# Performance work log

Hardware: AMD Instinct MI355X
Metric: run time of the kernel (lower is better)

Reference implementation:

```python
import jax, jax.numpy as jnp
import numpy as np
from jax import lax

# ---- model dims ----
NTOKEN = 60697
D_MODEL = 512
NLAYERS = 4
D_STATE = 16
D_CONV = 4
EXPAND = 2
D_INNER = EXPAND * D_MODEL      # 1024
DT_RANK = (D_MODEL + 15) // 16  # 32 (ceil(d_model/16), mamba default)
B_SZ = 4
SEQ = 2048
EPS = 1e-5


def setup_inputs() -> dict:
    key = jax.random.key(0)
    ks = jax.random.split(key, 16)
    s = 0.02
    src = jax.random.randint(ks[0], (B_SZ, SEQ), 0, NTOKEN)
    src_key_padding_mask = jnp.ones((B_SZ, SEQ), dtype=bool)
    emb_w = jax.random.normal(ks[1], (NTOKEN, D_MODEL), jnp.float32) * s
    enc_ln_w = jnp.ones((D_MODEL,), jnp.float32)
    enc_ln_b = jnp.zeros((D_MODEL,), jnp.float32)
    ln_w = jnp.ones((NLAYERS, D_MODEL), jnp.float32)
    ln_b = jnp.zeros((NLAYERS, D_MODEL), jnp.float32)
    in_proj_w = jax.random.normal(ks[2], (NLAYERS, 2 * D_INNER, D_MODEL), jnp.float32) * s
    conv_w = jax.random.normal(ks[3], (NLAYERS, D_INNER, D_CONV), jnp.float32) * 0.1
    conv_b = jnp.zeros((NLAYERS, D_INNER), jnp.float32)
    x_proj_w = jax.random.normal(ks[4], (NLAYERS, DT_RANK + 2 * D_STATE, D_INNER), jnp.float32) * s
    dt_proj_w = jax.random.normal(ks[5], (NLAYERS, D_INNER, DT_RANK), jnp.float32) * (DT_RANK ** -0.5)
    dt_proj_b = jax.random.uniform(ks[6], (NLAYERS, D_INNER), jnp.float32, -4.0, -2.0)
    # S4D real init: A = -[1..d_state], stored as log
    A_log = jnp.log(jnp.broadcast_to(jnp.arange(1, D_STATE + 1, dtype=jnp.float32),
                                     (NLAYERS, D_INNER, D_STATE)))
    D_skip = jnp.ones((NLAYERS, D_INNER), jnp.float32)
    out_proj_w = jax.random.normal(ks[7], (NLAYERS, D_MODEL, D_INNER), jnp.float32) * s / np.sqrt(NLAYERS)
    normf_w = jnp.ones((D_MODEL,), jnp.float32)
    normf_b = jnp.zeros((D_MODEL,), jnp.float32)
    return {
        'src': src, 'src_key_padding_mask': src_key_padding_mask,
        'emb_w': emb_w, 'enc_ln_w': enc_ln_w, 'enc_ln_b': enc_ln_b,
        'ln_w': ln_w, 'ln_b': ln_b, 'in_proj_w': in_proj_w,
        'conv_w': conv_w, 'conv_b': conv_b, 'x_proj_w': x_proj_w,
        'dt_proj_w': dt_proj_w, 'dt_proj_b': dt_proj_b,
        'A_log': A_log, 'D_skip': D_skip, 'out_proj_w': out_proj_w,
        'normf_w': normf_w, 'normf_b': normf_b,
    }


def _layer_norm(x, w, b, eps=EPS):
    mu = jnp.mean(x, axis=-1, keepdims=True)
    var = jnp.mean(jnp.square(x - mu), axis=-1, keepdims=True)
    return (x - mu) * lax.rsqrt(var + eps) * w + b


def _mamba_mixer(h, in_w, cw, cb, xw, dtw, dtb, A_log, D_skip, ow):
    B, L, _ = h.shape
    xz = h @ in_w.T                                   # [B,L,2*d_inner]
    x, z = jnp.split(xz, 2, axis=-1)
    # causal depthwise conv1d, kernel D_CONV
    xt = x.swapaxes(1, 2)                             # [B,d_inner,L]
    xp = jnp.pad(xt, ((0, 0), (0, 0), (D_CONV - 1, 0)))
    conv = cb[None, :, None]
    for k in range(D_CONV):
        conv = conv + cw[:, k][None, :, None] * xp[:, :, k:k + L]
    x = jax.nn.silu(conv).swapaxes(1, 2)              # [B,L,d_inner]
    xdbl = x @ xw.T                                   # [B,L,dt_rank+2*d_state]
    dt = jax.nn.softplus(xdbl[..., :DT_RANK] @ dtw.T + dtb)      # [B,L,d_inner]
    Bm = xdbl[..., DT_RANK:DT_RANK + D_STATE]                    # [B,L,d_state]
    Cm = xdbl[..., DT_RANK + D_STATE:]                           # [B,L,d_state]
    A = -jnp.exp(A_log)                               # [d_inner,d_state]

    def step(hst, inp):
        dt_t, b_t, c_t, x_t = inp                     # [B,d_inner],[B,d_state],[B,d_state],[B,d_inner]
        dA = jnp.exp(dt_t[..., None] * A)             # [B,d_inner,d_state]
        hst = dA * hst + (dt_t * x_t)[..., None] * b_t[:, None, :]
        y_t = jnp.einsum('bds,bs->bd', hst, c_t)
        return hst, y_t

    xs = (dt.swapaxes(0, 1), Bm.swapaxes(0, 1), Cm.swapaxes(0, 1), x.swapaxes(0, 1))
    h0 = jnp.zeros((B, D_INNER, D_STATE), dtype=h.dtype)
    _, ys = lax.scan(step, h0, xs)                    # ys: [L,B,d_inner]
    y = ys.swapaxes(0, 1) + x * D_skip
    y = y * jax.nn.silu(z)
    return y @ ow.T


def reference(src, src_key_padding_mask, emb_w, enc_ln_w, enc_ln_b, ln_w, ln_b,
              in_proj_w, conv_w, conv_b, x_proj_w, dt_proj_w, dt_proj_b,
              A_log, D_skip, out_proj_w, normf_w, normf_b):
    # GeneEncoder: embedding -> LayerNorm (dropout = identity in eval)
    hidden = _layer_norm(emb_w[src], enc_ln_w, enc_ln_b)
    residual = None
    for i in range(NLAYERS):  # prenorm Mamba Blocks
        residual = hidden if residual is None else hidden + residual
        hidden = _mamba_mixer(_layer_norm(residual, ln_w[i], ln_b[i]),
                              in_proj_w[i], conv_w[i], conv_b[i], x_proj_w[i],
                              dt_proj_w[i], dt_proj_b[i], A_log[i], D_skip[i],
                              out_proj_w[i])
    residual = hidden + residual
    return _layer_norm(residual, normf_w, normf_b)
```

## Files before the change

kernel.cpp:

```cpp
#include <hip/hip_runtime.h>
#include <hip/hip_bf16.h>
#include <math.h>

#define NTOKEN 60697
#define D_MODEL 512
#define NLAYERS 4
#define D_STATE 16
#define D_CONV 4
#define D_INNER 1024
#define DT_RANK 32
#define B_SZ 4
#define SEQ 2048
#define EPS 1e-5f
#define NROWS (B_SZ * SEQ)
#define CHUNK 128
#define NCHUNK (SEQ / CHUNK)

typedef __bf16 bf16_t;
typedef __attribute__((ext_vector_type(8))) __bf16 bfx8;
typedef __attribute__((ext_vector_type(4))) __bf16 bfx4;
typedef __attribute__((ext_vector_type(4))) float f32x4;


__device__ __forceinline__ float fast_sigmoid(float x) {
    return 1.0f / (1.0f + __expf(-x));
}
__device__ __forceinline__ float silu(float x) {
    return x * fast_sigmoid(x);
}
__device__ __forceinline__ float softplus_f(float x) {
    return (x > 20.0f) ? x : log1pf(__expf(x));
}

__device__ __forceinline__ void gload_lds16(const void* g, void* l) {
    __builtin_amdgcn_global_load_lds(
        (const __attribute__((address_space(1))) unsigned int*)g,
        (__attribute__((address_space(3))) unsigned int*)l, 16, 0, 0);
}

template <int CTRL>
__device__ __forceinline__ float dpp_fetch(float x) {
    int xi = __builtin_bit_cast(int, x);
    int yi = __builtin_amdgcn_update_dpp(0, xi, CTRL, 0xF, 0xF, true);
    return __builtin_bit_cast(float, yi);
}
__device__ __forceinline__ float dpp_sum16(float p) {
    p += dpp_fetch<0xB1>(p);
    p += dpp_fetch<0x4E>(p);
    p += dpp_fetch<0x141>(p);
    p += dpp_fetch<0x140>(p);
    return p;
}

__device__ __forceinline__ float blk_reduce_sum(float x, float* sbuf) {
#pragma unroll
    for (int m = 32; m >= 1; m >>= 1) x += __shfl_xor(x, m);
    int wid = threadIdx.x >> 6;
    if ((threadIdx.x & 63) == 0) sbuf[wid] = x;
    __syncthreads();
    float t = sbuf[0] + sbuf[1] + sbuf[2] + sbuf[3];
    __syncthreads();
    return t;
}

__global__ __launch_bounds__(256) void cast_bf16_kernel(
    const float* __restrict__ in, bf16_t* __restrict__ out, size_t n)
{
    size_t stride = (size_t)gridDim.x * 256 * 4;
    for (size_t i = ((size_t)blockIdx.x * 256 + threadIdx.x) * 4; i < n; i += stride) {
        float4 v = *reinterpret_cast<const float4*>(in + i);
        bfx4 o;
        o[0] = (bf16_t)v.x; o[1] = (bf16_t)v.y;
        o[2] = (bf16_t)v.z; o[3] = (bf16_t)v.w;
        *reinterpret_cast<bfx4*>(out + i) = o;
    }
}


__global__ __launch_bounds__(256) void embed_ln_kernel(
    const int* __restrict__ src, const float* __restrict__ emb,
    const float* __restrict__ w, const float* __restrict__ b,
    float* __restrict__ R)
{
    __shared__ float sbuf[4];
    int row = blockIdx.x;
    int tok = src[row];
    const float* e = emb + (size_t)tok * D_MODEL;
    int c0 = threadIdx.x, c1 = threadIdx.x + 256;
    float v0 = e[c0], v1 = e[c1];
    float mu = blk_reduce_sum(v0 + v1, sbuf) * (1.0f / D_MODEL);
    float d0 = v0 - mu, d1 = v1 - mu;
    float var = blk_reduce_sum(d0 * d0 + d1 * d1, sbuf) * (1.0f / D_MODEL);
    float rs = rsqrtf(var + EPS);
    size_t base = (size_t)row * D_MODEL;
    R[base + c0] = d0 * rs * w[c0] + b[c0];
    R[base + c1] = d1 * rs * w[c1] + b[c1];
}

__global__ __launch_bounds__(256) void add_ln_kernel(
    float* __restrict__ R, const float* __restrict__ Hadd,
    const float* __restrict__ w, const float* __restrict__ b,
    float* __restrict__ out, bf16_t* __restrict__ outb)
{
    __shared__ float sbuf[4];
    size_t base = (size_t)blockIdx.x * D_MODEL;
    int c0 = threadIdx.x, c1 = c0 + 256;
    float v0 = R[base + c0], v1 = R[base + c1];
    if (Hadd) {
        v0 += Hadd[base + c0];
        v1 += Hadd[base + c1];
        R[base + c0] = v0;
        R[base + c1] = v1;
    }
    float mu = blk_reduce_sum(v0 + v1, sbuf) * (1.0f / D_MODEL);
    float d0 = v0 - mu, d1 = v1 - mu;
    float var = blk_reduce_sum(d0 * d0 + d1 * d1, sbuf) * (1.0f / D_MODEL);
    float rs = rsqrtf(var + EPS);
    float o0 = d0 * rs * w[c0] + b[c0];
    float o1 = d1 * rs * w[c1] + b[c1];
    if (out) {
        out[base + c0] = o0;
        out[base + c1] = o1;
    }
    if (outb) {
        outb[base + c0] = (bf16_t)o0;
        outb[base + c1] = (bf16_t)o1;
    }
}

template <int EPI>
__global__ __launch_bounds__(256) void gemm_bf16_nt(
    const bf16_t* __restrict__ A, const bf16_t* __restrict__ B,
    float* __restrict__ C, int ldc, int K, const float* __restrict__ bias,
    const unsigned short* __restrict__ xcb_u16,
    unsigned short* __restrict__ dtx_u16,
    bf16_t* __restrict__ Cxb, bf16_t* __restrict__ Czb)
{
    __shared__ bf16_t As[128 * 32];
    __shared__ bf16_t Bs[128 * 32];
    int tid = threadIdx.x;
    int lane = tid & 63, wid = tid >> 6;
    int m0 = blockIdx.y * 128, n0 = blockIdx.x * 128;
    int wm = (wid >> 1) * 64, wn = (wid & 1) * 64;
    int c_lo = lane & 15;
    int khalf = lane >> 4;

    f32x4 acc[4][4];
#pragma unroll
    for (int i = 0; i < 4; i++)
#pragma unroll
        for (int j = 0; j < 4; j++)
            acc[i][j] = (f32x4){0.f, 0.f, 0.f, 0.f};

    for (int k0 = 0; k0 < K; k0 += 32) {
#pragma unroll
        for (int i = 0; i < 2; i++) {
            int c = i * 256 + tid;
            int row = c >> 2;
            int cb = (c & 3) * 16;
            int ldsoff = (i * 256 + wid * 64) * 16;
            gload_lds16((const char*)A + ((size_t)(m0 + row) * K + k0) * 2 + cb,
                        (char*)As + ldsoff);
            gload_lds16((const char*)B + ((size_t)(n0 + row) * K + k0) * 2 + cb,
                        (char*)Bs + ldsoff);
        }
        __syncthreads();

        bfx8 af[4], bfr[4];
#pragma unroll
        for (int i = 0; i < 4; i++) {
            af[i]  = *reinterpret_cast<const bfx8*>(As + (wm + i * 16 + c_lo) * 32 + khalf * 8);
            bfr[i] = *reinterpret_cast<const bfx8*>(Bs + (wn + i * 16 + c_lo) * 32 + khalf * 8);
        }
#pragma unroll
        for (int i = 0; i < 4; i++)
#pragma unroll
            for (int j = 0; j < 4; j++)
                acc[i][j] = __builtin_amdgcn_mfma_f32_16x16x32_bf16(af[i], bfr[j], acc[i][j], 0, 0, 0);
        __syncthreads();
    }

#pragma unroll
    for (int i = 0; i < 4; i++) {
#pragma unroll
        for (int j = 0; j < 4; j++) {
            int row0 = m0 + wm + i * 16 + khalf * 4;
            int col = n0 + wn + j * 16 + c_lo;
#pragma unroll
            for (int r = 0; r < 4; r++) {
                int row = row0 + r;
                float v = acc[i][j][r];
                if (EPI == 0) {
                    C[(size_t)row * ldc + col] = v;
                } else if (EPI == 2) {
                    v = softplus_f(v + bias[col]);
                    unsigned int db = (unsigned int)__builtin_bit_cast(unsigned short, (bf16_t)v);
                    unsigned int xb = (unsigned int)xcb_u16[(size_t)row * D_INNER + col];
                    *(unsigned int*)(dtx_u16 + (size_t)row * 2048 + 2 * col) = db | (xb << 16);
                } else if (EPI == 3) {
                    if (col < D_INNER) Cxb[(size_t)row * D_INNER + col] = (bf16_t)v;
                    else               Czb[(size_t)row * D_INNER + col - D_INNER] = (bf16_t)v;
                }
            }
        }
    }
}

__global__ __launch_bounds__(128) void gemm_xp_bf16(
    const bf16_t* __restrict__ A, const bf16_t* __restrict__ Bmat,
    bf16_t* __restrict__ XDlow, float* __restrict__ BCX, int K)
{
    __shared__ bf16_t As[64 * 32];
    __shared__ bf16_t Bs[64 * 32];
    int tid = threadIdx.x;
    int lane = tid & 63, w = tid >> 6;
    int m0 = blockIdx.x * 64;
    int wr0 = w * 32;
    int c_lo = lane & 15;
    int khalf = lane >> 4;

    f32x4 acc[2][4];
#pragma unroll
    for (int i = 0; i < 2; i++)
#pragma unroll
        for (int j = 0; j < 4; j++)
            acc[i][j] = (f32x4){0.f, 0.f, 0.f, 0.f};

    for (int k0 = 0; k0 < K; k0 += 32) {
#pragma unroll
        for (int call = 0; call < 2; call++) {
            int c = call * 128 + tid;
            int base = (call * 128 + w * 64) * 16;
            gload_lds16((const char*)A + ((size_t)(m0 + (c >> 2)) * K + k0) * 2 + (c & 3) * 16,
                        (char*)As + base);
            gload_lds16((const char*)Bmat + ((size_t)(c >> 2) * K + k0) * 2 + (c & 3) * 16,
                        (char*)Bs + base);
        }
        __syncthreads();

        bfx8 af[2], bfr[4];
#pragma unroll
        for (int i = 0; i < 2; i++)
            af[i] = *reinterpret_cast<const bfx8*>(As + (wr0 + i * 16 + c_lo) * 32 + khalf * 8);
#pragma unroll
        for (int j = 0; j < 4; j++)
            bfr[j] = *reinterpret_cast<const bfx8*>(Bs + (j * 16 + c_lo) * 32 + khalf * 8);
#pragma unroll
        for (int i = 0; i < 2; i++)
#pragma unroll
            for (int j = 0; j < 4; j++)
                acc[i][j] = __builtin_amdgcn_mfma_f32_16x16x32_bf16(af[i], bfr[j], acc[i][j], 0, 0, 0);
        __syncthreads();
    }

#pragma unroll
    for (int i = 0; i < 2; i++)
#pragma unroll
        for (int j = 0; j < 4; j++) {
            int row0 = m0 + wr0 + i * 16 + khalf * 4;
            int col = j * 16 + c_lo;
#pragma unroll
            for (int r = 0; r < 4; r++) {
                int row = row0 + r;
                float v = acc[i][j][r];
                if (col < DT_RANK) {
                    XDlow[(size_t)row * DT_RANK + col] = (bf16_t)v;
                } else {
                    int c2 = col - DT_RANK;
                    BCX[(size_t)row * 32 + 2 * (c2 & 15) + (c2 >> 4)] = v;
                }
            }
        }
}

__global__ __launch_bounds__(256) void conv_silu_kernel(
    const bf16_t* __restrict__ Xrawb, const float* __restrict__ cw,
    const float* __restrict__ cb, bf16_t* __restrict__ XCb)
{
    size_t gid = (size_t)blockIdx.x * 256 + threadIdx.x;
    int d = (int)(gid & (D_INNER - 1));
    size_t bt = gid >> 10;
    int t = (int)(bt & (SEQ - 1));
    float acc = cb[d];
#pragma unroll
    for (int k = 0; k < D_CONV; k++) {
        int tt = t + k - (D_CONV - 1);
        if (tt >= 0)
            acc += cw[d * D_CONV + k] * (float)Xrawb[(bt + (size_t)(k - (D_CONV - 1))) * D_INNER + d];
    }
    XCb[gid] = (bf16_t)silu(acc);
}

__device__ __forceinline__ void scan_stage(
    char* base, const unsigned int* __restrict__ DTXb,
    const float* __restrict__ BCX, size_t r0, int d0, int w, int lane)
{
    if (w < 2) {
        int cdt = w * 64 + lane;
        gload_lds16((const char*)DTXb + ((r0 + (cdt >> 2)) * 1024 + d0) * 4 + (cdt & 3) * 16,
                    base + w * 1024);
        int cbc = 128 + w * 64;
        gload_lds16((const char*)BCX + (r0 + ((cbc + lane) >> 3)) * 128 + ((cbc + lane) & 7) * 16,
                    base + 2048 + cbc * 16);
    } else {
        int cbc = (w - 2) * 64;
        gload_lds16((const char*)BCX + (r0 + ((cbc + lane) >> 3)) * 128 + ((cbc + lane) & 7) * 16,
                    base + 2048 + cbc * 16);
    }
}

__global__ __launch_bounds__(256) void scan_pA_kernel(
    const unsigned int* __restrict__ DTXb, const float* __restrict__ BCX,
    const float* __restrict__ A_log,
    float* __restrict__ DcB, float* __restrict__ UcB)
{
    __shared__ __align__(16) char lds[2][6144];
    const int tid = threadIdx.x;
    const int w = tid >> 6, lane = tid & 63;
    const int s = tid & 15, dl = tid >> 4;
    const int b = blockIdx.x >> 6;
    const int d0 = (blockIdx.x & 63) * 16;
    const int c = blockIdx.y;
    const int d = d0 + dl;
    const float Av = -__expf(A_log[d * D_STATE + s]);
    const size_t bbase = (size_t)b * SEQ;
    const int tstart = c * CHUNK;

    float h = 0.f, cum = 0.f;
    scan_stage(lds[0], DTXb, BCX, bbase + tstart, d0, w, lane);
    __syncthreads();
    int cur = 0;
    for (int t0 = 0; t0 < CHUNK; t0 += 32) {
        if (t0 + 32 < CHUNK)
            scan_stage(lds[cur ^ 1], DTXb, BCX, bbase + tstart + t0 + 32, d0, w, lane);
        const char* L = lds[cur];
#pragma unroll
        for (int kk = 0; kk < 32; kk++) {
            unsigned int pk = *(const unsigned int*)(L + kk * 64 + dl * 4);
            float dtv = __builtin_bit_cast(float, pk << 16);
            float xv  = __builtin_bit_cast(float, pk & 0xFFFF0000u);
            float bv  = *(const float*)(L + 2048 + kk * 128 + s * 8);
            float e = __expf(dtv * Av);
            h = fmaf(e, h, dtv * xv * bv);
            cum += dtv;
        }
        __syncthreads();
        cur ^= 1;
    }
    size_t cb64 = ((size_t)c * B_SZ + b) * D_INNER + d;
    UcB[cb64 * 16 + s] = h;
    if (s == 0) DcB[cb64] = cum;
}

__global__ __launch_bounds__(256) void scan_p2_kernel(
    const float* __restrict__ A_log, const float* __restrict__ DcB,
    const float* __restrict__ UcB, float* __restrict__ HcB)
{
    int tid = threadIdx.x;
    int s = tid & 15, dl = tid >> 4;
    int chain = blockIdx.x * 16 + dl;
    int b = chain >> 10, d = chain & 1023;
    float Av = -__expf(A_log[d * D_STATE + s]);
    float Hv = 0.f;
    for (int c = 0; c < NCHUNK; c++) {
        size_t base = ((size_t)c * B_SZ + b) * D_INNER + d;
        HcB[base * 16 + s] = Hv;
        Hv = __expf(Av * DcB[base]) * Hv + UcB[base * 16 + s];
    }
}

__global__ __launch_bounds__(256) void scan_pB_kernel(
    const unsigned int* __restrict__ DTXb, const float* __restrict__ BCX,
    const float* __restrict__ HcB, const float* __restrict__ A_log,
    const bf16_t* __restrict__ Zbufb, const float* __restrict__ Dskip,
    bf16_t* __restrict__ XCb)
{
    __shared__ __align__(16) char lds[2][6144];
    __shared__ float ytile[32][17];
    const int tid = threadIdx.x;
    const int w = tid >> 6, lane = tid & 63;
    const int s = tid & 15, dl = tid >> 4;
    const int b = blockIdx.x >> 6;
    const int d0 = (blockIdx.x & 63) * 16;
    const int c = blockIdx.y;
    const int d = d0 + dl;
    const float Av = -__expf(A_log[d * D_STATE + s]);
    const size_t bbase = (size_t)b * SEQ;
    const int tstart = c * CHUNK;

    float h = HcB[(((size_t)c * B_SZ + b) * D_INNER + d) * 16 + s];

    const int tl  = tid >> 3;
    const int dlo = (tid * 2) & 15;
    const float dsk0 = Dskip[d0 + dlo];
    const float dsk1 = Dskip[d0 + dlo + 1];

    scan_stage(lds[0], DTXb, BCX, bbase + tstart, d0, w, lane);
    __syncthreads();
    int cur = 0;
    for (int t0 = 0; t0 < CHUNK; t0 += 32) {
        if (t0 + 32 < CHUNK)
            scan_stage(lds[cur ^ 1], DTXb, BCX, bbase + tstart + t0 + 32, d0, w, lane);
        const char* L = lds[cur];
#pragma unroll
        for (int half = 0; half < 2; half++) {
            float yhold = 0.f;
#pragma unroll
            for (int k = 0; k < 16; k++) {
                int kk = half * 16 + k;
                unsigned int pk = *(const unsigned int*)(L + kk * 64 + dl * 4);
                float dtv = __builtin_bit_cast(float, pk << 16);
                float xv  = __builtin_bit_cast(float, pk & 0xFFFF0000u);
                float2 bc = *(const float2*)(L + 2048 + kk * 128 + s * 8);
                float e = __expf(dtv * Av);
                h = fmaf(e, h, dtv * xv * bc.x);
                float p = dpp_sum16(h * bc.y);
                if (s == k) yhold = p;
            }
            ytile[half * 16 + s][dl] = yhold;
        }
        __syncthreads();

        {
            int t = tstart + t0 + tl;
            size_t row = (bbase + t) * (size_t)D_INNER + d0 + dlo;
            float y0 = ytile[tl][dlo];
            float y1 = ytile[tl][dlo + 1];
            unsigned int xw = *(const unsigned int*)(XCb + row);
            float x0 = __builtin_bit_cast(float, xw << 16);
            float x1 = __builtin_bit_cast(float, xw & 0xFFFF0000u);
            unsigned int zw = *(const unsigned int*)(Zbufb + row);
            float z0 = __builtin_bit_cast(float, zw << 16);
            float z1 = __builtin_bit_cast(float, zw & 0xFFFF0000u);
            float g0 = (y0 + x0 * dsk0) * silu(z0);
            float g1 = (y1 + x1 * dsk1) * silu(z1);
            unsigned int o = (unsigned int)__builtin_bit_cast(unsigned short, (bf16_t)g0)
                           | ((unsigned int)__builtin_bit_cast(unsigned short, (bf16_t)g1) << 16);
            *(unsigned int*)(XCb + row) = o;
        }
        __syncthreads();
        cur ^= 1;
    }
}


extern "C" void kernel_launch(void* const* d_in, const int* in_sizes, int n_in,
                              void* d_out, int out_size, void* d_ws, size_t ws_size,
                              hipStream_t stream) {
    const int*   src       = (const int*)d_in[0];
    const float* emb_w     = (const float*)d_in[2];
    const float* enc_ln_w  = (const float*)d_in[3];
    const float* enc_ln_b  = (const float*)d_in[4];
    const float* ln_w      = (const float*)d_in[5];
    const float* ln_b      = (const float*)d_in[6];
    const float* in_proj_w = (const float*)d_in[7];
    const float* conv_w    = (const float*)d_in[8];
    const float* conv_b    = (const float*)d_in[9];
    const float* x_proj_w  = (const float*)d_in[10];
    const float* dt_proj_w = (const float*)d_in[11];
    const float* dt_proj_b = (const float*)d_in[12];
    const float* A_log     = (const float*)d_in[13];
    const float* D_skip    = (const float*)d_in[14];
    const float* out_proj_w= (const float*)d_in[15];
    const float* normf_w   = (const float*)d_in[16];
    const float* normf_b   = (const float*)d_in[17];
    float* out = (float*)d_out;

    float* R    = (float*)d_ws;
    float* H    = R    + (size_t)NROWS * D_MODEL;
    float* BCX  = H    + (size_t)NROWS * D_MODEL;
    float* DcB  = BCX  + (size_t)NROWS * 32;
    float* UcB  = DcB  + (size_t)NCHUNK * B_SZ * D_INNER;
    float* HcB  = UcB  + (size_t)NCHUNK * B_SZ * D_INNER * D_STATE;
    bf16_t* Hb    = (bf16_t*)(HcB + (size_t)NCHUNK * B_SZ * D_INNER * D_STATE);
    bf16_t* Xrawb = Hb    + (size_t)NROWS * D_MODEL;
    bf16_t* Zbufb = Xrawb + (size_t)NROWS * D_INNER;
    bf16_t* XCb   = Zbufb + (size_t)NROWS * D_INNER;
    bf16_t* XDlow = XCb   + (size_t)NROWS * D_INNER;
    unsigned short* DTXb = (unsigned short*)(XDlow + (size_t)NROWS * DT_RANK);
    bf16_t* Wib   = (bf16_t*)(DTXb + (size_t)NROWS * 2048);
    bf16_t* Wob   = Wib   + (size_t)NLAYERS * 2 * D_INNER * D_MODEL;
    bf16_t* xpb   = Wob   + (size_t)NLAYERS * D_MODEL * D_INNER;
    bf16_t* dtwb  = xpb   + (size_t)NLAYERS * 64 * D_INNER;

    cast_bf16_kernel<<<2048, 256, 0, stream>>>(in_proj_w, Wib, (size_t)NLAYERS * 2 * D_INNER * D_MODEL);
    cast_bf16_kernel<<<2048, 256, 0, stream>>>(out_proj_w, Wob, (size_t)NLAYERS * D_MODEL * D_INNER);
    cast_bf16_kernel<<<256, 256, 0, stream>>>(x_proj_w, xpb, (size_t)NLAYERS * 64 * D_INNER);
    cast_bf16_kernel<<<128, 256, 0, stream>>>(dt_proj_w, dtwb, (size_t)NLAYERS * D_INNER * DT_RANK);

    embed_ln_kernel<<<NROWS, 256, 0, stream>>>(src, emb_w, enc_ln_w, enc_ln_b, R);

    for (int L = 0; L < NLAYERS; L++) {
        const float* AlogL = A_log + (size_t)L * D_INNER * D_STATE;

        add_ln_kernel<<<NROWS, 256, 0, stream>>>(
            R, (L == 0) ? nullptr : H, ln_w + L * D_MODEL, ln_b + L * D_MODEL,
            nullptr, Hb);

        gemm_bf16_nt<3><<<dim3(16, 64), 256, 0, stream>>>(
            Hb, Wib + (size_t)L * 2 * D_INNER * D_MODEL, nullptr, 0, D_MODEL,
            nullptr, nullptr, nullptr, Xrawb, Zbufb);

        conv_silu_kernel<<<(NROWS * D_INNER) / 256, 256, 0, stream>>>(
            Xrawb, conv_w + (size_t)L * D_INNER * D_CONV, conv_b + (size_t)L * D_INNER, XCb);

        gemm_xp_bf16<<<NROWS / 64, 128, 0, stream>>>(
            XCb, xpb + (size_t)L * 64 * D_INNER, XDlow, BCX, D_INNER);

        gemm_bf16_nt<2><<<dim3(8, 64), 256, 0, stream>>>(
            XDlow, dtwb + (size_t)L * D_INNER * DT_RANK, nullptr, 0, DT_RANK,
            dt_proj_b + (size_t)L * D_INNER, (const unsigned short*)XCb, DTXb,
            nullptr, nullptr);

        scan_pA_kernel<<<dim3(B_SZ * 64, NCHUNK), 256, 0, stream>>>(
            (const unsigned int*)DTXb, BCX, AlogL, DcB, UcB);
        scan_p2_kernel<<<256, 256, 0, stream>>>(AlogL, DcB, UcB, HcB);
        scan_pB_kernel<<<dim3(B_SZ * 64, NCHUNK), 256, 0, stream>>>(
            (const unsigned int*)DTXb, BCX, HcB, AlogL, Zbufb,
            D_skip + (size_t)L * D_INNER, XCb);

        gemm_bf16_nt<0><<<dim3(4, 64), 256, 0, stream>>>(
            XCb, Wob + (size_t)L * D_MODEL * D_INNER, H, D_MODEL, D_INNER,
            nullptr, nullptr, nullptr, nullptr, nullptr);
    }

    add_ln_kernel<<<NROWS, 256, 0, stream>>>(R, H, normf_w, normf_b, out, nullptr);
}
```

Measured before the change: 1.091 ms.

## Pack scan inputs as bf16 row-pairs, precompute dt*x, use exp2

The dt epilogue now stores dt and dt*x as bf16 pairs, interleaved by row pairs. The x_proj epilogue stores B and C as bf16 pairs in the same row-pair layout instead of fp32. The scan kernels stage 64 timesteps per LDS buffer with one 16-byte load per thread, read two timesteps per uint2, and use raw v_exp_f32 with A pre-scaled by log2e. This is meant to halve B/C traffic, cut per-step multiplies and exp cost, and make staging simpler. In exchange B, C and dt*x lose precision by being rounded to bf16 before the recurrence.

```diff
diff --git a/kernel.cpp b/kernel.cpp
--- a/kernel.cpp
+++ b/kernel.cpp
@@ -15,6 +15,7 @@
 #define NROWS (B_SZ * SEQ)
 #define CHUNK 128
 #define NCHUNK (SEQ / CHUNK)
+#define LOG2E 1.44269504f
 
 typedef __bf16 bf16_t;
 typedef __attribute__((ext_vector_type(8))) __bf16 bfx8;
@@ -30,6 +31,20 @@
 }
 __device__ __forceinline__ float softplus_f(float x) {
     return (x > 20.0f) ? x : log1pf(__expf(x));
+}
+__device__ __forceinline__ float exp2_fast(float x) {
+    float r;
+    asm("v_exp_f32 %0, %1" : "=v"(r) : "v"(x));
+    return r;
+}
+__device__ __forceinline__ unsigned int bf16bits(float v) {
+    return (unsigned int)__builtin_bit_cast(unsigned short, (bf16_t)v);
+}
+__device__ __forceinline__ float lo16f(unsigned int u) {
+    return __builtin_bit_cast(float, u << 16);
+}
+__device__ __forceinline__ float hi16f(unsigned int u) {
+    return __builtin_bit_cast(float, u & 0xFFFF0000u);
 }
 
 __device__ __forceinline__ void gload_lds16(const void* g, void* l) {
@@ -133,7 +148,7 @@
     const bf16_t* __restrict__ A, const bf16_t* __restrict__ B,
     float* __restrict__ C, int ldc, int K, const float* __restrict__ bias,
     const unsigned short* __restrict__ xcb_u16,
-    unsigned short* __restrict__ dtx_u16,
+    unsigned int* __restrict__ dtx_u32,
     bf16_t* __restrict__ Cxb, bf16_t* __restrict__ Czb)
 {
     __shared__ bf16_t As[128 * 32];
@@ -194,9 +209,9 @@
                     C[(size_t)row * ldc + col] = v;
                 } else if (EPI == 2) {
                     v = softplus_f(v + bias[col]);
-                    unsigned int db = (unsigned int)__builtin_bit_cast(unsigned short, (bf16_t)v);
-                    unsigned int xb = (unsigned int)xcb_u16[(size_t)row * D_INNER + col];
-                    *(unsigned int*)(dtx_u16 + (size_t)row * 2048 + 2 * col) = db | (xb << 16);
+                    float xf = lo16f((unsigned int)xcb_u16[(size_t)row * D_INNER + col]);
+                    unsigned int u = bf16bits(v) | (bf16bits(v * xf) << 16);
+                    dtx_u32[(size_t)(row >> 1) * 2048 + col * 2 + (row & 1)] = u;
                 } else if (EPI == 3) {
                     if (col < D_INNER) Cxb[(size_t)row * D_INNER + col] = (bf16_t)v;
                     else               Czb[(size_t)row * D_INNER + col - D_INNER] = (bf16_t)v;
@@ -208,7 +223,7 @@
 
 __global__ __launch_bounds__(128) void gemm_xp_bf16(
     const bf16_t* __restrict__ A, const bf16_t* __restrict__ Bmat,
-    bf16_t* __restrict__ XDlow, float* __restrict__ BCX, int K)
+    bf16_t* __restrict__ XDlow, unsigned int* __restrict__ BCb, int K)
 {
     __shared__ bf16_t As[64 * 32];
     __shared__ bf16_t Bs[64 * 32];
@@ -254,23 +269,17 @@
     }
 
 #pragma unroll
-    for (int i = 0; i < 2; i++)
-#pragma unroll
-        for (int j = 0; j < 4; j++) {
-            int row0 = m0 + wr0 + i * 16 + khalf * 4;
-            int col = j * 16 + c_lo;
-#pragma unroll
-            for (int r = 0; r < 4; r++) {
-                int row = row0 + r;
-                float v = acc[i][j][r];
-                if (col < DT_RANK) {
-                    XDlow[(size_t)row * DT_RANK + col] = (bf16_t)v;
-                } else {
-                    int c2 = col - DT_RANK;
-                    BCX[(size_t)row * 32 + 2 * (c2 & 15) + (c2 >> 4)] = v;
-                }
-            }
-        }
+    for (int i = 0; i < 2; i++) {
+        int row0 = m0 + wr0 + i * 16 + khalf * 4;
+#pragma unroll
+        for (int r = 0; r < 4; r++) {
+            int row = row0 + r;
+            XDlow[(size_t)row * DT_RANK + c_lo]      = (bf16_t)acc[i][0][r];
+            XDlow[(size_t)row * DT_RANK + 16 + c_lo] = (bf16_t)acc[i][1][r];
+            unsigned int u = bf16bits(acc[i][2][r]) | (bf16bits(acc[i][3][r]) << 16);
+            BCb[(size_t)(row >> 1) * 32 + c_lo * 2 + (row & 1)] = u;
+        }
+    }
 }
 
 __global__ __launch_bounds__(256) void conv_silu_kernel(
@@ -291,58 +300,54 @@
     XCb[gid] = (bf16_t)silu(acc);
 }
 
-__device__ __forceinline__ void scan_stage(
-    char* base, const unsigned int* __restrict__ DTXb,
-    const float* __restrict__ BCX, size_t r0, int d0, int w, int lane)
-{
-    if (w < 2) {
-        int cdt = w * 64 + lane;
-        gload_lds16((const char*)DTXb + ((r0 + (cdt >> 2)) * 1024 + d0) * 4 + (cdt & 3) * 16,
-                    base + w * 1024);
-        int cbc = 128 + w * 64;
-        gload_lds16((const char*)BCX + (r0 + ((cbc + lane) >> 3)) * 128 + ((cbc + lane) & 7) * 16,
-                    base + 2048 + cbc * 16);
-    } else {
-        int cbc = (w - 2) * 64;
-        gload_lds16((const char*)BCX + (r0 + ((cbc + lane) >> 3)) * 128 + ((cbc + lane) & 7) * 16,
-                    base + 2048 + cbc * 16);
-    }
+__device__ __forceinline__ void scan_stage64(
+    char* base, const unsigned int* __restrict__ DTXp,
+    const unsigned int* __restrict__ BCp, size_t rowpair0, int d0, int tid)
+{
+    gload_lds16(DTXp + (rowpair0 + (size_t)(tid >> 3)) * 2048 + d0 * 2 + (tid & 7) * 4,
+                base + tid * 16);
+    gload_lds16(BCp + rowpair0 * 32 + tid * 4, base + 4096 + tid * 16);
 }
 
 __global__ __launch_bounds__(256) void scan_pA_kernel(
-    const unsigned int* __restrict__ DTXb, const float* __restrict__ BCX,
+    const unsigned int* __restrict__ DTXb, const unsigned int* __restrict__ BCb,
     const float* __restrict__ A_log,
     float* __restrict__ DcB, float* __restrict__ UcB)
 {
-    __shared__ __align__(16) char lds[2][6144];
+    __shared__ __align__(16) char lds[2][8192];
     const int tid = threadIdx.x;
-    const int w = tid >> 6, lane = tid & 63;
     const int s = tid & 15, dl = tid >> 4;
     const int b = blockIdx.x >> 6;
     const int d0 = (blockIdx.x & 63) * 16;
     const int c = blockIdx.y;
     const int d = d0 + dl;
-    const float Av = -__expf(A_log[d * D_STATE + s]);
+    const float Av2 = -__expf(A_log[d * D_STATE + s]) * LOG2E;
     const size_t bbase = (size_t)b * SEQ;
     const int tstart = c * CHUNK;
 
     float h = 0.f, cum = 0.f;
-    scan_stage(lds[0], DTXb, BCX, bbase + tstart, d0, w, lane);
+    scan_stage64(lds[0], DTXb, BCb, (bbase + tstart) >> 1, d0, tid);
     __syncthreads();
     int cur = 0;
-    for (int t0 = 0; t0 < CHUNK; t0 += 32) {
-        if (t0 + 32 < CHUNK)
-            scan_stage(lds[cur ^ 1], DTXb, BCX, bbase + tstart + t0 + 32, d0, w, lane);
+    for (int t0 = 0; t0 < CHUNK; t0 += 64) {
+        if (t0 + 64 < CHUNK)
+            scan_stage64(lds[cur ^ 1], DTXb, BCb, (bbase + tstart + t0 + 64) >> 1, d0, tid);
         const char* L = lds[cur];
 #pragma unroll
-        for (int kk = 0; kk < 32; kk++) {
-            unsigned int pk = *(const unsigned int*)(L + kk * 64 + dl * 4);
-            float dtv = __builtin_bit_cast(float, pk << 16);
-            float xv  = __builtin_bit_cast(float, pk & 0xFFFF0000u);
-            float bv  = *(const float*)(L + 2048 + kk * 128 + s * 8);
-            float e = __expf(dtv * Av);
-            h = fmaf(e, h, dtv * xv * bv);
-            cum += dtv;
+        for (int kk2 = 0; kk2 < 32; kk2++) {
+            uint2 dp = *(const uint2*)(L + kk2 * 128 + dl * 8);
+            uint2 bp = *(const uint2*)(L + 4096 + kk2 * 128 + s * 8);
+#pragma unroll
+            for (int j = 0; j < 2; j++) {
+                unsigned int pk = j ? dp.y : dp.x;
+                unsigned int bk = j ? bp.y : bp.x;
+                float dtv = lo16f(pk);
+                float ux  = hi16f(pk);
+                float bv  = lo16f(bk);
+                float e = exp2_fast(dtv * Av2);
+                h = fmaf(e, h, ux * bv);
+                cum += dtv;
+            }
         }
         __syncthreads();
         cur ^= 1;
@@ -370,21 +375,20 @@
 }
 
 __global__ __launch_bounds__(256) void scan_pB_kernel(
-    const unsigned int* __restrict__ DTXb, const float* __restrict__ BCX,
+    const unsigned int* __restrict__ DTXb, const unsigned int* __restrict__ BCb,
     const float* __restrict__ HcB, const float* __restrict__ A_log,
     const bf16_t* __restrict__ Zbufb, const float* __restrict__ Dskip,
     bf16_t* __restrict__ XCb)
 {
-    __shared__ __align__(16) char lds[2][6144];
+    __shared__ __align__(16) char lds[2][8192];
     __shared__ float ytile[32][17];
     const int tid = threadIdx.x;
-    const int w = tid >> 6, lane = tid & 63;
     const int s = tid & 15, dl = tid >> 4;
     const int b = blockIdx.x >> 6;
     const int d0 = (blockIdx.x & 63) * 16;
     const int c = blockIdx.y;
     const int d = d0 + dl;
-    const float Av = -__expf(A_log[d * D_STATE + s]);
+    const float Av2 = -__expf(A_log[d * D_STATE + s]) * LOG2E;
     const size_t bbase = (size_t)b * SEQ;
     const int tstart = c * CHUNK;
 
@@ -395,50 +399,56 @@
     const float dsk0 = Dskip[d0 + dlo];
     const float dsk1 = Dskip[d0 + dlo + 1];
 
-    scan_stage(lds[0], DTXb, BCX, bbase + tstart, d0, w, lane);
+    scan_stage64(lds[0], DTXb, BCb, (bbase + tstart) >> 1, d0, tid);
     __syncthreads();
     int cur = 0;
-    for (int t0 = 0; t0 < CHUNK; t0 += 32) {
-        if (t0 + 32 < CHUNK)
-            scan_stage(lds[cur ^ 1], DTXb, BCX, bbase + tstart + t0 + 32, d0, w, lane);
+    for (int t0 = 0; t0 < CHUNK; t0 += 64) {
+        if (t0 + 64 < CHUNK)
+            scan_stage64(lds[cur ^ 1], DTXb, BCb, (bbase + tstart + t0 + 64) >> 1, d0, tid);
         const char* L = lds[cur];
 #pragma unroll
-        for (int half = 0; half < 2; half++) {
-            float yhold = 0.f;
-#pragma unroll
-            for (int k = 0; k < 16; k++) {
-                int kk = half * 16 + k;
-                unsigned int pk = *(const unsigned int*)(L + kk * 64 + dl * 4);
-                float dtv = __builtin_bit_cast(float, pk << 16);
-                float xv  = __builtin_bit_cast(float, pk & 0xFFFF0000u);
-                float2 bc = *(const float2*)(L + 2048 + kk * 128 + s * 8);
-                float e = __expf(dtv * Av);
-                h = fmaf(e, h, dtv * xv * bc.x);
-                float p = dpp_sum16(h * bc.y);
-                if (s == k) yhold = p;
+        for (int g = 0; g < 2; g++) {
+#pragma unroll
+            for (int half = 0; half < 2; half++) {
+                float yhold = 0.f;
+#pragma unroll
+                for (int k8 = 0; k8 < 8; k8++) {
+                    int kk2 = g * 16 + half * 8 + k8;
+                    uint2 dp = *(const uint2*)(L + kk2 * 128 + dl * 8);
+                    uint2 bp = *(const uint2*)(L + 4096 + kk2 * 128 + s * 8);
+#pragma unroll
+                    for (int j = 0; j < 2; j++) {
+                        unsigned int pk = j ? dp.y : dp.x;
+                        unsigned int bk = j ? bp.y : bp.x;
+                        float dtv = lo16f(pk);
+                        float ux  = hi16f(pk);
+                        float bv  = lo16f(bk);
+                        float cv  = hi16f(bk);
+                        float e = exp2_fast(dtv * Av2);
+                        h = fmaf(e, h, ux * bv);
+                        float p = dpp_sum16(h * cv);
+                        if (s == k8 * 2 + j + half * 0) {  }
+                        int k16 = k8 * 2 + j;
+                        if (s == k16) yhold = p;
+                    }
+                }
+                ytile[half * 16 + s][dl] = yhold;
             }
-            ytile[half * 16 + s][dl] = yhold;
-        }
-        __syncthreads();
-
-        {
-            int t = tstart + t0 + tl;
-            size_t row = (bbase + t) * (size_t)D_INNER + d0 + dlo;
-            float y0 = ytile[tl][dlo];
-            float y1 = ytile[tl][dlo + 1];
-            unsigned int xw = *(const unsigned int*)(XCb + row);
-            float x0 = __builtin_bit_cast(float, xw << 16);
-            float x1 = __builtin_bit_cast(float, xw & 0xFFFF0000u);
-            unsigned int zw = *(const unsigned int*)(Zbufb + row);
-            float z0 = __builtin_bit_cast(float, zw << 16);
-            float z1 = __builtin_bit_cast(float, zw & 0xFFFF0000u);
-            float g0 = (y0 + x0 * dsk0) * silu(z0);
-            float g1 = (y1 + x1 * dsk1) * silu(z1);
-            unsigned int o = (unsigned int)__builtin_bit_cast(unsigned short, (bf16_t)g0)
-                           | ((unsigned int)__builtin_bit_cast(unsigned short, (bf16_t)g1) << 16);
-            *(unsigned int*)(XCb + row) = o;
-        }
-        __syncthreads();
+            __syncthreads();
+            {
+                int t = tstart + t0 + g * 32 + tl;
+                size_t row = (bbase + t) * (size_t)D_INNER + d0 + dlo;
+                float y0 = ytile[tl][dlo];
+                float y1 = ytile[tl][dlo + 1];
+                unsigned int xw = *(const unsigned int*)(XCb + row);
+                unsigned int zw = *(const unsigned int*)(Zbufb + row);
+                float g0 = (y0 + lo16f(xw) * dsk0) * silu(lo16f(zw));
+                float g1 = (y1 + hi16f(xw) * dsk1) * silu(hi16f(zw));
+                unsigned int o = bf16bits(g0) | (bf16bits(g1) << 16);
+                *(unsigned int*)(XCb + row) = o;
+            }
+            __syncthreads();
+        }
         cur ^= 1;
     }
 }
@@ -468,17 +478,17 @@
 
     float* R    = (float*)d_ws;
     float* H    = R    + (size_t)NROWS * D_MODEL;
-    float* BCX  = H    + (size_t)NROWS * D_MODEL;
-    float* DcB  = BCX  + (size_t)NROWS * 32;
+    float* DcB  = H    + (size_t)NROWS * D_MODEL;
     float* UcB  = DcB  + (size_t)NCHUNK * B_SZ * D_INNER;
     float* HcB  = UcB  + (size_t)NCHUNK * B_SZ * D_INNER * D_STATE;
-    bf16_t* Hb    = (bf16_t*)(HcB + (size_t)NCHUNK * B_SZ * D_INNER * D_STATE);
+    unsigned int* BCb = (unsigned int*)(HcB + (size_t)NCHUNK * B_SZ * D_INNER * D_STATE);
+    unsigned int* DTXb = BCb + (size_t)(NROWS / 2) * 32;
+    bf16_t* Hb    = (bf16_t*)(DTXb + (size_t)(NROWS / 2) * 2048);
     bf16_t* Xrawb = Hb    + (size_t)NROWS * D_MODEL;
     bf16_t* Zbufb = Xrawb + (size_t)NROWS * D_INNER;
     bf16_t* XCb   = Zbufb + (size_t)NROWS * D_INNER;
     bf16_t* XDlow = XCb   + (size_t)NROWS * D_INNER;
-    unsigned short* DTXb = (unsigned short*)(XDlow + (size_t)NROWS * DT_RANK);
-    bf16_t* Wib   = (bf16_t*)(DTXb + (size_t)NROWS * 2048);
+    bf16_t* Wib   = XDlow + (size_t)NROWS * DT_RANK;
     bf16_t* Wob   = Wib   + (size_t)NLAYERS * 2 * D_INNER * D_MODEL;
     bf16_t* xpb   = Wob   + (size_t)NLAYERS * D_MODEL * D_INNER;
     bf16_t* dtwb  = xpb   + (size_t)NLAYERS * 64 * D_INNER;
@@ -505,7 +515,7 @@
             Xrawb, conv_w + (size_t)L * D_INNER * D_CONV, conv_b + (size_t)L * D_INNER, XCb);
 
         gemm_xp_bf16<<<NROWS / 64, 128, 0, stream>>>(
-            XCb, xpb + (size_t)L * 64 * D_INNER, XDlow, BCX, D_INNER);
+            XCb, xpb + (size_t)L * 64 * D_INNER, XDlow, BCb, D_INNER);
 
         gemm_bf16_nt<2><<<dim3(8, 64), 256, 0, stream>>>(
             XDlow, dtwb + (size_t)L * D_INNER * DT_RANK, nullptr, 0, DT_RANK,
@@ -513,11 +523,10 @@
             nullptr, nullptr);
 
         scan_pA_kernel<<<dim3(B_SZ * 64, NCHUNK), 256, 0, stream>>>(
-            (const unsigned int*)DTXb, BCX, AlogL, DcB, UcB);
+            DTXb, BCb, AlogL, DcB, UcB);
         scan_p2_kernel<<<256, 256, 0, stream>>>(AlogL, DcB, UcB, HcB);
         scan_pB_kernel<<<dim3(B_SZ * 64, NCHUNK), 256, 0, stream>>>(
-            (const unsigned int*)DTXb, BCX, HcB, AlogL, Zbufb,
-            D_skip + (size_t)L * D_INNER, XCb);
+            DTXb, BCb, HcB, AlogL, Zbufb, D_skip + (size_t)L * D_INNER, XCb);
 
         gemm_bf16_nt<0><<<dim3(4, 64), 256, 0, stream>>>(
             XCb, Wob + (size_t)L * D_MODEL * D_INNER, H, D_MODEL, D_INNER,
```

Measured after the change: 1.084 ms. Within noise of the previous version (-0.7%).
